# Kernel tuning notes

Hardware: AMD Instinct MI355X
Metric: run time of the kernel (lower is better)

The kernel has to match this reference:

```python
import jax, jax.numpy as jnp
import numpy as np

N = 2000
E = 128
H = 8
DH = E // H
K = 32  # max_neighbors
CLAMP = 1e4


def _sanitize(t):
    t = jnp.nan_to_num(t, nan=0.0, posinf=CLAMP, neginf=-CLAMP)
    return jnp.clip(t, -CLAMP, CLAMP)


def _layernorm(h, g, b, eps=1e-5):
    mu = h.mean(-1, keepdims=True)
    var = ((h - mu) ** 2).mean(-1, keepdims=True)
    return (h - mu) * jax.lax.rsqrt(var + eps) * g + b


def setup_inputs() -> dict:
    key = jax.random.key(0)
    ks = jax.random.split(key, 8)
    x = jax.random.normal(ks[0], (N, E), dtype=jnp.float32)
    coords9 = jax.random.normal(ks[1], (N, 9), dtype=jnp.float32)
    prompt_signal = jax.random.normal(ks[2], (E,), dtype=jnp.float32)
    pe_w = jax.random.normal(ks[3], (3, 32), dtype=jnp.float32) / np.sqrt(3.0)
    pe_b = jnp.zeros((32,), jnp.float32)
    pe_g = jnp.ones((32,), jnp.float32)
    pe_bt = jnp.zeros((32,), jnp.float32)
    in_w = jax.random.normal(ks[4], (3 * E, E), dtype=jnp.float32) / np.sqrt(E)
    in_b = jnp.zeros((3 * E,), jnp.float32)
    out_w = jax.random.normal(ks[5], (E, E), dtype=jnp.float32) / np.sqrt(E)
    out_b = jnp.zeros((E,), jnp.float32)
    return {"x": x, "coords9": coords9, "prompt_signal": prompt_signal,
            "pe_w": pe_w, "pe_b": pe_b, "pe_g": pe_g, "pe_bt": pe_bt,
            "in_w": in_w, "in_b": in_b, "out_w": out_w, "out_b": out_b}


def reference(x, coords9, prompt_signal, pe_w, pe_b, pe_g, pe_bt, in_w, in_b, out_w, out_b):
    n = x.shape[0]
    verts = coords9.reshape(n, 3, 3)
    cent = verts.mean(axis=1)  # (N,3)

    # pairwise centroid distances (only geo-relation channel that affects the output;
    # cos_angles/area_ratios/boundary_sharing feed geo_bias which is dead code in forward)
    diff = cent[:, None, :] - cent[None, :, :]
    dist = jnp.sqrt(jnp.sum(diff * diff, axis=-1) + 1e-20)  # (N,N)

    # positional encoder: Linear(3,32) -> GELU(exact) -> LayerNorm(32)
    pe = jax.nn.gelu(cent @ pe_w + pe_b, approximate=False)
    pe = _layernorm(pe, pe_g, pe_bt)  # (N,32)

    prompt_enhanced = x + prompt_signal[None, :]
    pos_enhanced = jnp.concatenate([prompt_enhanced[:, : 3 * E // 4], pe], axis=-1)  # (N,128)

    # top-K nearest neighbors -> additive attention mask (0 for kept, -inf-like otherwise)
    _, topk_idx = jax.lax.top_k(-dist, K)  # (N,K) smallest distances
    big_neg = jnp.float32(-1e9)
    attn_mask = jnp.full((n, n), big_neg, dtype=jnp.float32)
    attn_mask = attn_mask.at[jnp.arange(n)[:, None], topk_idx].set(0.0)

    # nn.MultiheadAttention (self-attention, eval mode -> no dropout)
    qkv = pos_enhanced @ in_w.T + in_b  # (N,3E)
    q, k, v = jnp.split(qkv, 3, axis=-1)
    q = q.reshape(n, H, DH).transpose(1, 0, 2)  # (H,N,DH)
    k = k.reshape(n, H, DH).transpose(1, 0, 2)
    v = v.reshape(n, H, DH).transpose(1, 0, 2)
    scores = jnp.einsum('hnd,hmd->hnm', q, k) / np.sqrt(DH) + attn_mask[None]
    probs = jax.nn.softmax(scores, axis=-1)
    o = jnp.einsum('hnm,hmd->hnd', probs, v)  # (H,N,DH)
    o = o.transpose(1, 0, 2).reshape(n, E)
    out = o @ out_w.T + out_b
    return _sanitize(out)
```

## Files before the change

kernel.cpp:

```cpp
#include <hip/hip_runtime.h>
#include <math.h>

#define N_NODES 2000
#define E_DIM   128
#define QKV_W   384
#define LDA     36

__global__ __launch_bounds__(256) void prep_qkv_kernel(
    const float* __restrict__ x, const float* __restrict__ coords9,
    const float* __restrict__ ps, const float* __restrict__ pe_w,
    const float* __restrict__ pe_b, const float* __restrict__ pe_g,
    const float* __restrict__ pe_bt, const float* __restrict__ in_w,
    const float* __restrict__ in_b,
    float* __restrict__ cx_, float* __restrict__ cy_, float* __restrict__ cz_,
    float* __restrict__ qkv)
{
    __shared__ __align__(16) float As[E_DIM * LDA];
    int tid = threadIdx.x;
    int rt = blockIdx.x / 3, ct = blockIdx.x % 3;
    int rbase = rt * 32, cbase = ct * 128;
    int g = tid >> 5, lane = tid & 31;

    #pragma unroll
    for (int rr = 0; rr < 4; ++rr) {
        int rl = rr * 8 + g;
        int row = rbase + rl;
        bool vr = (row < N_NODES);
        float cx = 0.f, cy = 0.f, cz = 0.f;
        if (vr) {
            const float* c9 = coords9 + row * 9;
            cx = (c9[0] + c9[3] + c9[6]) * (1.0f / 3.0f);
            cy = (c9[1] + c9[4] + c9[7]) * (1.0f / 3.0f);
            cz = (c9[2] + c9[5] + c9[8]) * (1.0f / 3.0f);
        }
        if (ct == 0 && vr && lane == 0) { cx_[row] = cx; cy_[row] = cy; cz_[row] = cz; }

        #pragma unroll
        for (int k = 0; k < 3; ++k) {
            int c = lane + 32 * k;
            float v = vr ? (x[row * E_DIM + c] + ps[c]) : 0.f;
            As[c * LDA + rl] = v;
        }

        int j = lane;
        float h = cx * pe_w[j] + cy * pe_w[32 + j] + cz * pe_w[64 + j] + pe_b[j];
        float ge = 0.5f * h * (1.0f + erff(h * 0.7071067811865476f));
        float s = ge;
        #pragma unroll
        for (int m = 16; m >= 1; m >>= 1) s += __shfl_xor(s, m);
        float mu = s * (1.0f / 32.0f);
        float d = ge - mu;
        float v2 = d * d;
        #pragma unroll
        for (int m = 16; m >= 1; m >>= 1) v2 += __shfl_xor(v2, m);
        float var = v2 * (1.0f / 32.0f);
        float y = d * (1.0f / sqrtf(var + 1e-5f)) * pe_g[j] + pe_bt[j];
        As[(96 + j) * LDA + rl] = vr ? y : 0.f;
    }
    __syncthreads();

    int cg = tid & 31, rg = tid >> 5;
    int c0 = cbase + cg * 4, r0 = rg * 4;
    float acc[4][4];
    #pragma unroll
    for (int i = 0; i < 4; ++i)
        #pragma unroll
        for (int jj = 0; jj < 4; ++jj) acc[i][jj] = 0.f;

    for (int k0 = 0; k0 < 128; k0 += 4) {
        float4 a0 = *(const float4*)&As[(k0 + 0) * LDA + r0];
        float4 a1 = *(const float4*)&As[(k0 + 1) * LDA + r0];
        float4 a2 = *(const float4*)&As[(k0 + 2) * LDA + r0];
        float4 a3 = *(const float4*)&As[(k0 + 3) * LDA + r0];
        #pragma unroll
        for (int ci = 0; ci < 4; ++ci) {
            float4 b = *(const float4*)&in_w[(c0 + ci) * E_DIM + k0];
            acc[0][ci] += a0.x * b.x + a1.x * b.y + a2.x * b.z + a3.x * b.w;
            acc[1][ci] += a0.y * b.x + a1.y * b.y + a2.y * b.z + a3.y * b.w;
            acc[2][ci] += a0.z * b.x + a1.z * b.y + a2.z * b.z + a3.z * b.w;
            acc[3][ci] += a0.w * b.x + a1.w * b.y + a2.w * b.z + a3.w * b.w;
        }
    }

    #pragma unroll
    for (int ri = 0; ri < 4; ++ri) {
        int row = rbase + r0 + ri;
        if (row < N_NODES) {
            float4 o4;
            o4.x = acc[ri][0] + in_b[c0 + 0];
            o4.y = acc[ri][1] + in_b[c0 + 1];
            o4.z = acc[ri][2] + in_b[c0 + 2];
            o4.w = acc[ri][3] + in_b[c0 + 3];
            *(float4*)&qkv[row * QKV_W + c0] = o4;
        }
    }
}

__device__ __forceinline__ float sanitize(float v)
{
    v = (v == v) ? v : 0.f;
    return fminf(fmaxf(v, -1e4f), 1e4f);
}

__global__ __launch_bounds__(256) void attn_proj_kernel(
    const float* __restrict__ cx_, const float* __restrict__ cy_,
    const float* __restrict__ cz_, const float* __restrict__ qkv,
    const float* __restrict__ out_w, const float* __restrict__ out_b,
    float* __restrict__ out)
{
    __shared__ unsigned int hist[256];
    __shared__ float wMin[4], wMax[4];
    __shared__ int sh_b, sh_nless, sh_sel, sh_eq;
    __shared__ int waveSum[4];
    __shared__ int topk[32];
    __shared__ int eqIdx[256];
    __shared__ unsigned int eqKey[256];
    __shared__ __align__(16) float qs[128];
    __shared__ float pr[256];
    __shared__ __align__(16) float os[128];

    int tid = threadIdx.x;
    int row = blockIdx.x;
    int lane = tid & 63, wid = tid >> 6;

    float cix = cx_[row], ciy = cy_[row], ciz = cz_[row];
    unsigned int kbits[8];
    int bins[8];
    bool valid[8];
    float lmin = __int_as_float(0x7f800000);
    float lmax = __int_as_float(0xff800000);
    {
        #pragma clang fp contract(off)
        #pragma unroll
        for (int l = 0; l < 8; ++l) {
            int j = tid + 256 * l;
            valid[l] = (j < N_NODES);
            float key = __int_as_float(0x7f800000);
            if (valid[l]) {
                float dx = cix - cx_[j];
                float dy = ciy - cy_[j];
                float dz = ciz - cz_[j];
                float a = dx * dx;
                float b = dy * dy;
                float c = dz * dz;
                float d2 = ((a + b) + c) + 1e-20f;
                key = sqrtf(d2);
                lmin = fminf(lmin, key);
                lmax = fmaxf(lmax, key);
            }
            kbits[l] = __float_as_uint(key);
        }
    }

    #pragma unroll
    for (int m = 32; m >= 1; m >>= 1) {
        lmin = fminf(lmin, __shfl_xor(lmin, m));
        lmax = fmaxf(lmax, __shfl_xor(lmax, m));
    }
    if (lane == 0) { wMin[wid] = lmin; wMax[wid] = lmax; }
    hist[tid] = 0u;
    if (tid == 0) { sh_sel = 0; sh_eq = 0; }
    __syncthreads();
    float lo = fminf(fminf(wMin[0], wMin[1]), fminf(wMin[2], wMin[3]));
    float hi = fmaxf(fmaxf(wMax[0], wMax[1]), fmaxf(wMax[2], wMax[3]));
    float scale = 255.0f / fmaxf(hi - lo, 1e-30f);

    #pragma unroll
    for (int l = 0; l < 8; ++l) {
        int bin = 255;
        if (valid[l]) {
            float key = __uint_as_float(kbits[l]);
            bin = (int)((key - lo) * scale);
            bin = min(max(bin, 0), 255);
            atomicAdd(&hist[bin], 1u);
        }
        bins[l] = bin;
    }
    __syncthreads();

    int h = (int)hist[tid];
    int incl = h;
    #pragma unroll
    for (int dd = 1; dd < 64; dd <<= 1) {
        int u = __shfl_up(incl, dd);
        if (lane >= dd) incl += u;
    }
    if (lane == 63) waveSum[wid] = incl;
    __syncthreads();
    int off = 0;
    for (int w = 0; w < wid; ++w) off += waveSum[w];
    int cum = incl + off;
    if (cum >= 32 && (cum - h) < 32) {
        sh_b = tid;
        sh_nless = cum - h;
    }
    __syncthreads();

    int b = sh_b;
    int req = 32 - sh_nless;

    #pragma unroll
    for (int l = 0; l < 8; ++l) {
        if (valid[l]) {
            int bin = bins[l];
            int j = tid + 256 * l;
            if (bin < b) {
                int p = atomicAdd(&sh_sel, 1);
                topk[p] = j;
            } else if (bin == b) {
                int e = atomicAdd(&sh_eq, 1);
                if (e < 256) { eqIdx[e] = j; eqKey[e] = kbits[l]; }
            }
        }
    }
    if (tid < 128) qs[tid] = qkv[row * QKV_W + tid];
    __syncthreads();

    int eq = min(sh_eq, 256);
    if (tid < eq) {
        int myIdx = eqIdx[tid];
        unsigned int myKey = eqKey[tid];
        int rank = 0;
        for (int u = 0; u < eq; ++u) {
            unsigned int ku = eqKey[u];
            rank += (ku < myKey || (ku == myKey && eqIdx[u] < myIdx)) ? 1 : 0;
        }
        if (rank < req) {
            int p = atomicAdd(&sh_sel, 1);
            topk[p] = myIdx;
        }
    }
    __syncthreads();

    {
        int hh = tid >> 5, j = tid & 31;
        int jj = topk[j];
        const float4* kp = (const float4*)&qkv[jj * QKV_W + 128 + hh * 16];
        const float4* qp = (const float4*)&qs[hh * 16];
        float s = 0.f;
        #pragma unroll
        for (int i = 0; i < 4; ++i) {
            float4 kv = kp[i], qv = qp[i];
            s += qv.x * kv.x + qv.y * kv.y + qv.z * kv.z + qv.w * kv.w;
        }
        s *= 0.25f;
        float m = s;
        #pragma unroll
        for (int msk = 16; msk >= 1; msk >>= 1) m = fmaxf(m, __shfl_xor(m, msk));
        float p = expf(s - m);
        float su = p;
        #pragma unroll
        for (int msk = 16; msk >= 1; msk >>= 1) su += __shfl_xor(su, msk);
        pr[tid] = p / su;
    }
    __syncthreads();

    if (tid < 128) {
        int hh = tid >> 4;
        float acc = 0.f;
        #pragma unroll
        for (int j = 0; j < 32; ++j) {
            int jj = topk[j];
            acc += pr[hh * 32 + j] * qkv[jj * QKV_W + 256 + tid];
        }
        os[tid] = acc;
    }
    __syncthreads();

    if (tid < 128) {
        const float* wr = out_w + tid * E_DIM;
        float a = 0.f;
        #pragma unroll
        for (int e = 0; e < 128; e += 4) {
            float4 w4 = *(const float4*)&wr[e];
            float4 o4 = *(const float4*)&os[e];
            a += o4.x * w4.x + o4.y * w4.y + o4.z * w4.z + o4.w * w4.w;
        }
        out[row * E_DIM + tid] = sanitize(a + out_b[tid]);
    }
}

extern "C" void kernel_launch(void* const* d_in, const int* in_sizes, int n_in,
                              void* d_out, int out_size, void* d_ws, size_t ws_size,
                              hipStream_t stream)
{
    const float* x      = (const float*)d_in[0];
    const float* coords = (const float*)d_in[1];
    const float* ps     = (const float*)d_in[2];
    const float* pe_w   = (const float*)d_in[3];
    const float* pe_b   = (const float*)d_in[4];
    const float* pe_g   = (const float*)d_in[5];
    const float* pe_bt  = (const float*)d_in[6];
    const float* in_w   = (const float*)d_in[7];
    const float* in_b   = (const float*)d_in[8];
    const float* out_w  = (const float*)d_in[9];
    const float* out_b  = (const float*)d_in[10];
    float* out = (float*)d_out;

    float* ws  = (float*)d_ws;
    float* cxp = ws;
    float* cyp = ws + 2048;
    float* czp = ws + 4096;
    float* qkvb = ws + 6144;

    prep_qkv_kernel<<<189, 256, 0, stream>>>(x, coords, ps, pe_w, pe_b, pe_g, pe_bt,
                                             in_w, in_b, cxp, cyp, czp, qkvb);
    attn_proj_kernel<<<2000, 256, 0, stream>>>(cxp, cyp, czp, qkvb, out_w, out_b, out);
}
```

Measured before the change: 123.4 us.

## Split output projection into a separate tiled GEMM kernel

Moves the per-row output projection out of the attention kernel into a new kernel that computes 32-row tiles with register blocking. The attention kernel now writes its per-row attention output to a workspace buffer. Each out_w element is then reused across 32 rows instead of being re-read by every row's block, and the attention kernel's tail with its extra barrier goes away. In exchange it adds a kernel launch, a global round trip for the intermediate, and a small grid of only 63 blocks for the projection.

```diff
diff --git a/kernel.cpp b/kernel.cpp
--- a/kernel.cpp
+++ b/kernel.cpp
@@ -105,8 +105,7 @@
 __global__ __launch_bounds__(256) void attn_proj_kernel(
     const float* __restrict__ cx_, const float* __restrict__ cy_,
     const float* __restrict__ cz_, const float* __restrict__ qkv,
-    const float* __restrict__ out_w, const float* __restrict__ out_b,
-    float* __restrict__ out)
+    float* __restrict__ osb)
 {
     __shared__ unsigned int hist[256];
     __shared__ float wMin[4], wMax[4];
@@ -117,7 +116,6 @@
     __shared__ unsigned int eqKey[256];
     __shared__ __align__(16) float qs[128];
     __shared__ float pr[256];
-    __shared__ __align__(16) float os[128];
 
     int tid = threadIdx.x;
     int row = blockIdx.x;
@@ -263,20 +261,66 @@
             int jj = topk[j];
             acc += pr[hh * 32 + j] * qkv[jj * QKV_W + 256 + tid];
         }
-        os[tid] = acc;
-    }
-    __syncthreads();
-
-    if (tid < 128) {
-        const float* wr = out_w + tid * E_DIM;
-        float a = 0.f;
-        #pragma unroll
-        for (int e = 0; e < 128; e += 4) {
-            float4 w4 = *(const float4*)&wr[e];
-            float4 o4 = *(const float4*)&os[e];
-            a += o4.x * w4.x + o4.y * w4.y + o4.z * w4.z + o4.w * w4.w;
-        }
-        out[row * E_DIM + tid] = sanitize(a + out_b[tid]);
+        osb[row * E_DIM + tid] = acc;
+    }
+}
+
+__global__ __launch_bounds__(256) void out_proj_kernel(
+    const float* __restrict__ os_, const float* __restrict__ out_w,
+    const float* __restrict__ out_b, float* __restrict__ out)
+{
+    __shared__ __align__(16) float As[E_DIM * LDA];
+    int tid = threadIdx.x;
+    int rbase = blockIdx.x * 32;
+    int g = tid >> 5, lane = tid & 31;
+
+    #pragma unroll
+    for (int rr = 0; rr < 4; ++rr) {
+        int rl = rr * 8 + g;
+        int row = rbase + rl;
+        bool vr = (row < N_NODES);
+        #pragma unroll
+        for (int k = 0; k < 4; ++k) {
+            int c = lane + 32 * k;
+            As[c * LDA + rl] = vr ? os_[row * E_DIM + c] : 0.f;
+        }
+    }
+    __syncthreads();
+
+    int cg = tid & 31, rg = tid >> 5;
+    int c0 = cg * 4, r0 = rg * 4;
+    float acc[4][4];
+    #pragma unroll
+    for (int i = 0; i < 4; ++i)
+        #pragma unroll
+        for (int jj = 0; jj < 4; ++jj) acc[i][jj] = 0.f;
+
+    for (int k0 = 0; k0 < 128; k0 += 4) {
+        float4 a0 = *(const float4*)&As[(k0 + 0) * LDA + r0];
+        float4 a1 = *(const float4*)&As[(k0 + 1) * LDA + r0];
+        float4 a2 = *(const float4*)&As[(k0 + 2) * LDA + r0];
+        float4 a3 = *(const float4*)&As[(k0 + 3) * LDA + r0];
+        #pragma unroll
+        for (int ci = 0; ci < 4; ++ci) {
+            float4 b = *(const float4*)&out_w[(c0 + ci) * E_DIM + k0];
+            acc[0][ci] += a0.x * b.x + a1.x * b.y + a2.x * b.z + a3.x * b.w;
+            acc[1][ci] += a0.y * b.x + a1.y * b.y + a2.y * b.z + a3.y * b.w;
+            acc[2][ci] += a0.z * b.x + a1.z * b.y + a2.z * b.z + a3.z * b.w;
+            acc[3][ci] += a0.w * b.x + a1.w * b.y + a2.w * b.z + a3.w * b.w;
+        }
+    }
+
+    #pragma unroll
+    for (int ri = 0; ri < 4; ++ri) {
+        int row = rbase + r0 + ri;
+        if (row < N_NODES) {
+            float4 o4;
+            o4.x = sanitize(acc[ri][0] + out_b[c0 + 0]);
+            o4.y = sanitize(acc[ri][1] + out_b[c0 + 1]);
+            o4.z = sanitize(acc[ri][2] + out_b[c0 + 2]);
+            o4.w = sanitize(acc[ri][3] + out_b[c0 + 3]);
+            *(float4*)&out[row * E_DIM + c0] = o4;
+        }
     }
 }
 
@@ -302,8 +346,10 @@
     float* cyp = ws + 2048;
     float* czp = ws + 4096;
     float* qkvb = ws + 6144;
+    float* osb  = ws + 774144;
 
     prep_qkv_kernel<<<189, 256, 0, stream>>>(x, coords, ps, pe_w, pe_b, pe_g, pe_bt,
                                              in_w, in_b, cxp, cyp, czp, qkvb);
-    attn_proj_kernel<<<2000, 256, 0, stream>>>(cxp, cyp, czp, qkvb, out_w, out_b, out);
-}
+    attn_proj_kernel<<<2000, 256, 0, stream>>>(cxp, cyp, czp, qkvb, osb);
+    out_proj_kernel<<<63, 256, 0, stream>>>(osb, out_w, out_b, out);
+}
```

Result: slower. 129.8 us (+5.2%).

## Pack centroids as float4, transpose out_w for coalescing, split histogram atomics

Applied to the files above, without the earlier changes.

Centroids are now stored as a single float4 array instead of three separate arrays, so each neighbor distance needs one vector load. The prep kernel gets 16 extra blocks that write a transposed copy of out_w, which makes the output projection's weight reads coalesced across threads. The per-row histogram is split into two copies by wave parity to reduce LDS atomic contention. The costs are extra workspace, 16 extra blocks, and an additional global write of the transposed weights.

```diff
diff --git a/kernel.cpp b/kernel.cpp
--- a/kernel.cpp
+++ b/kernel.cpp
@@ -5,18 +5,32 @@
 #define E_DIM   128
 #define QKV_W   384
 #define LDA     36
+#define GEMM_BLOCKS 189
 
 __global__ __launch_bounds__(256) void prep_qkv_kernel(
     const float* __restrict__ x, const float* __restrict__ coords9,
     const float* __restrict__ ps, const float* __restrict__ pe_w,
     const float* __restrict__ pe_b, const float* __restrict__ pe_g,
     const float* __restrict__ pe_bt, const float* __restrict__ in_w,
-    const float* __restrict__ in_b,
-    float* __restrict__ cx_, float* __restrict__ cy_, float* __restrict__ cz_,
-    float* __restrict__ qkv)
+    const float* __restrict__ in_b, const float* __restrict__ out_w,
+    float4* __restrict__ cw, float* __restrict__ qkv,
+    float* __restrict__ out_wT)
 {
     __shared__ __align__(16) float As[E_DIM * LDA];
     int tid = threadIdx.x;
+
+    if (blockIdx.x >= GEMM_BLOCKS) {
+        int bid2 = blockIdx.x - GEMM_BLOCKS;
+        int g2 = tid >> 5, lane2 = tid & 31;
+        int k = bid2 * 8 + g2;
+        #pragma unroll
+        for (int m = 0; m < 4; ++m) {
+            int e = lane2 + 32 * m;
+            out_wT[k * 128 + e] = out_w[e * 128 + k];
+        }
+        return;
+    }
+
     int rt = blockIdx.x / 3, ct = blockIdx.x % 3;
     int rbase = rt * 32, cbase = ct * 128;
     int g = tid >> 5, lane = tid & 31;
@@ -33,7 +47,10 @@
             cy = (c9[1] + c9[4] + c9[7]) * (1.0f / 3.0f);
             cz = (c9[2] + c9[5] + c9[8]) * (1.0f / 3.0f);
         }
-        if (ct == 0 && vr && lane == 0) { cx_[row] = cx; cy_[row] = cy; cz_[row] = cz; }
+        if (ct == 0 && vr && lane == 0) {
+            float4 c4; c4.x = cx; c4.y = cy; c4.z = cz; c4.w = 0.f;
+            cw[row] = c4;
+        }
 
         #pragma unroll
         for (int k = 0; k < 3; ++k) {
@@ -103,12 +120,11 @@
 }
 
 __global__ __launch_bounds__(256) void attn_proj_kernel(
-    const float* __restrict__ cx_, const float* __restrict__ cy_,
-    const float* __restrict__ cz_, const float* __restrict__ qkv,
-    const float* __restrict__ out_w, const float* __restrict__ out_b,
+    const float4* __restrict__ cw, const float* __restrict__ qkv,
+    const float* __restrict__ out_wT, const float* __restrict__ out_b,
     float* __restrict__ out)
 {
-    __shared__ unsigned int hist[256];
+    __shared__ unsigned int hist[512];
     __shared__ float wMin[4], wMax[4];
     __shared__ int sh_b, sh_nless, sh_sel, sh_eq;
     __shared__ int waveSum[4];
@@ -123,7 +139,8 @@
     int row = blockIdx.x;
     int lane = tid & 63, wid = tid >> 6;
 
-    float cix = cx_[row], ciy = cy_[row], ciz = cz_[row];
+    float4 ci = cw[row];
+    float cix = ci.x, ciy = ci.y, ciz = ci.z;
     unsigned int kbits[8];
     int bins[8];
     bool valid[8];
@@ -137,9 +154,10 @@
             valid[l] = (j < N_NODES);
             float key = __int_as_float(0x7f800000);
             if (valid[l]) {
-                float dx = cix - cx_[j];
-                float dy = ciy - cy_[j];
-                float dz = ciz - cz_[j];
+                float4 cj = cw[j];
+                float dx = cix - cj.x;
+                float dy = ciy - cj.y;
+                float dz = ciz - cj.z;
                 float a = dx * dx;
                 float b = dy * dy;
                 float c = dz * dz;
@@ -159,12 +177,14 @@
     }
     if (lane == 0) { wMin[wid] = lmin; wMax[wid] = lmax; }
     hist[tid] = 0u;
+    hist[tid + 256] = 0u;
     if (tid == 0) { sh_sel = 0; sh_eq = 0; }
     __syncthreads();
     float lo = fminf(fminf(wMin[0], wMin[1]), fminf(wMin[2], wMin[3]));
     float hi = fmaxf(fmaxf(wMax[0], wMax[1]), fmaxf(wMax[2], wMax[3]));
     float scale = 255.0f / fmaxf(hi - lo, 1e-30f);
 
+    unsigned int hsel = (wid & 1) << 8;
     #pragma unroll
     for (int l = 0; l < 8; ++l) {
         int bin = 255;
@@ -172,13 +192,13 @@
             float key = __uint_as_float(kbits[l]);
             bin = (int)((key - lo) * scale);
             bin = min(max(bin, 0), 255);
-            atomicAdd(&hist[bin], 1u);
+            atomicAdd(&hist[hsel + bin], 1u);
         }
         bins[l] = bin;
     }
     __syncthreads();
 
-    int h = (int)hist[tid];
+    int h = (int)(hist[tid] + hist[tid + 256]);
     int incl = h;
     #pragma unroll
     for (int dd = 1; dd < 64; dd <<= 1) {
@@ -268,13 +288,13 @@
     __syncthreads();
 
     if (tid < 128) {
-        const float* wr = out_w + tid * E_DIM;
         float a = 0.f;
         #pragma unroll
-        for (int e = 0; e < 128; e += 4) {
-            float4 w4 = *(const float4*)&wr[e];
-            float4 o4 = *(const float4*)&os[e];
-            a += o4.x * w4.x + o4.y * w4.y + o4.z * w4.z + o4.w * w4.w;
+        for (int k = 0; k < 128; k += 4) {
+            a += os[k + 0] * out_wT[(k + 0) * 128 + tid]
+               + os[k + 1] * out_wT[(k + 1) * 128 + tid]
+               + os[k + 2] * out_wT[(k + 2) * 128 + tid]
+               + os[k + 3] * out_wT[(k + 3) * 128 + tid];
         }
         out[row * E_DIM + tid] = sanitize(a + out_b[tid]);
     }
@@ -297,13 +317,13 @@
     const float* out_b  = (const float*)d_in[10];
     float* out = (float*)d_out;
 
-    float* ws  = (float*)d_ws;
-    float* cxp = ws;
-    float* cyp = ws + 2048;
-    float* czp = ws + 4096;
-    float* qkvb = ws + 6144;
-
-    prep_qkv_kernel<<<189, 256, 0, stream>>>(x, coords, ps, pe_w, pe_b, pe_g, pe_bt,
-                                             in_w, in_b, cxp, cyp, czp, qkvb);
-    attn_proj_kernel<<<2000, 256, 0, stream>>>(cxp, cyp, czp, qkvb, out_w, out_b, out);
+    float* ws    = (float*)d_ws;
+    float4* cw   = (float4*)ws;
+    float* qkvb  = ws + 8192;
+    float* owT   = ws + 8192 + 768000;
+
+    prep_qkv_kernel<<<GEMM_BLOCKS + 16, 256, 0, stream>>>(
+        x, coords, ps, pe_w, pe_b, pe_g, pe_bt, in_w, in_b, out_w,
+        cw, qkvb, owT);
+    attn_proj_kernel<<<2000, 256, 0, stream>>>(cw, qkvb, owT, out_b, out);
 }
```

After: 113.4 us. 8.0% less time.
